# Kernel optimization log

Hardware: AMD Instinct MI355X
Metric: run time of the kernel (lower is better)

## Reference

```python
import jax, jax.numpy as jnp
import numpy as np

N, E = 50000, 800000
F_IN, HID, HEADS, OUT = 128, 32, 4, 16
NEG_SLOPE = 0.2  # PyG GATConv default leaky_relu slope


def segment_softmax(logits, seg, n):
    # numerically stable softmax over edges grouped by destination node
    m = jax.ops.segment_max(logits, seg, num_segments=n)          # [N,H]
    m = jnp.where(jnp.isfinite(m), m, 0.0)                        # guard empty segments
    e = jnp.exp(logits - m[seg])                                  # [E,H]
    s = jax.ops.segment_sum(e, seg, num_segments=n)               # [N,H]
    return e / (s[seg] + 1e-16)


def gat_conv(x, W, a_src, a_dst, bias, src, dst, concat):
    H, C = a_src.shape
    n = x.shape[0]
    h = (x @ W).reshape(n, H, C)                                  # [N,H,C]
    alpha_src = jnp.einsum('nhc,hc->nh', h, a_src)                # [N,H]
    alpha_dst = jnp.einsum('nhc,hc->nh', h, a_dst)                # [N,H]
    e = jax.nn.leaky_relu(alpha_src[src] + alpha_dst[dst], NEG_SLOPE)  # [E,H]
    alpha = segment_softmax(e, dst, n)                            # [E,H]
    msg = h[src] * alpha[:, :, None]                              # [E,H,C]
    out = jax.ops.segment_sum(msg, dst, num_segments=n)           # [N,H,C]
    out = out.reshape(n, H * C) if concat else out.mean(axis=1)
    return out + bias


def setup_inputs() -> dict:
    key = jax.random.key(0)
    ks = jax.random.split(key, 12)
    s = 0.1  # keep attention logits in a sane range
    return {
        'x': jax.random.normal(ks[0], (N, F_IN), jnp.float32),
        'edge_index': jax.random.randint(ks[1], (2, E), 0, N),
        'Wemb': jax.random.normal(ks[2], (F_IN, HID), jnp.float32) * s,
        'bemb': jnp.zeros((HID,), jnp.float32),
        'W1': jax.random.normal(ks[3], (HID, HEADS * HID), jnp.float32) * s,
        'a_src1': jax.random.normal(ks[4], (HEADS, HID), jnp.float32) * s,
        'a_dst1': jax.random.normal(ks[5], (HEADS, HID), jnp.float32) * s,
        'b1': jnp.zeros((HEADS * HID,), jnp.float32),
        'W2': jax.random.normal(ks[6], (HEADS * HID, HEADS * OUT), jnp.float32) * s,
        'a_src2': jax.random.normal(ks[7], (HEADS, OUT), jnp.float32) * s,
        'a_dst2': jax.random.normal(ks[8], (HEADS, OUT), jnp.float32) * s,
        'b2': jnp.zeros((OUT,), jnp.float32),
    }


def reference(x, edge_index, Wemb, bemb, W1, a_src1, a_dst1, b1, W2, a_src2, a_dst2, b2):
    src, dst = edge_index[0], edge_index[1]
    h = x @ Wemb + bemb  # dropout layers are identity at inference
    h = jax.nn.elu(gat_conv(h, W1, a_src1, a_dst1, b1, src, dst, True))
    h = gat_conv(h, W2, a_src2, a_dst2, b2, src, dst, False)
    return jax.nn.log_softmax(h, axis=1)
```

## Files before the change

kernel.cpp:

```cpp
#include <hip/hip_runtime.h>

#define N_NODES 50000
#define N_EDGES 800000
#define F_IN    128
#define HID     32
#define HEADS   4
#define OUT_C   16

#define NBKT 196
#define CAP  5120
#define EPB  4096
#define NB64 782

typedef __attribute__((ext_vector_type(8))) short bf16x8;
typedef __attribute__((ext_vector_type(4))) float f32x4;

__device__ __forceinline__ unsigned short f2bf(float f) {
    unsigned int u = __float_as_uint(f);
    u += 0x7FFFu + ((u >> 16) & 1u);
    return (unsigned short)(u >> 16);
}
__device__ __forceinline__ float bf_lo(unsigned int u) { return __uint_as_float(u << 16); }
__device__ __forceinline__ float bf_hi(unsigned int u) { return __uint_as_float(u & 0xFFFF0000u); }
__device__ __forceinline__ float bf2f(unsigned short s) {
    return __uint_as_float(((unsigned int)s) << 16);
}

__device__ __forceinline__ float edge_w(float asv, float adv) {
    float v = asv + adv;
    v = (v > 0.f) ? v : 0.2f * v;
    return __expf(v);
}

__global__ __launch_bounds__(256) void k_F1(const float* __restrict__ x,
                                            const float* __restrict__ Wemb,
                                            const float* __restrict__ bemb,
                                            const float* __restrict__ W1,
                                            const float* __restrict__ a_src,
                                            const float* __restrict__ a_dst,
                                            unsigned short* __restrict__ h0b,
                                            float* __restrict__ as, float* __restrict__ ad,
                                            const int* __restrict__ ei,
                                            int* __restrict__ gcnt,
                                            unsigned int* __restrict__ pairs) {
    __shared__ unsigned short xsb[64][136];
    __shared__ unsigned short wet[HID][136];
    __shared__ float bl[HID];
    __shared__ float vs[HID][4];
    __shared__ float vd[HID][4];
    __shared__ int hist[NBKT];
    __shared__ int base[NBKT];
    int t = threadIdx.x;
    if (blockIdx.x < NB64) {
        int node0 = blockIdx.x * 64;
        if (t < HID) bl[t] = bemb[t];
        {
            int k = (t & 127) >> 2, h = t & 3;
            const float* wrow = W1 + k * 128 + h * 32;
            const float* arow = ((t < 128) ? a_src : a_dst) + h * 32;
            float accv = 0.f;
            #pragma unroll
            for (int c2 = 0; c2 < 32; c2++) accv += wrow[c2] * arow[c2];
            if (t < 128) vs[k][h] = accv; else vd[k][h] = accv;
        }
        #pragma unroll
        for (int it = 0; it < 4; it++) {
            int idx = it * 256 + t;
            int k = idx >> 3, c4 = idx & 7;
            float4 w = *(const float4*)(Wemb + k * HID + c4 * 4);
            wet[c4 * 4 + 0][k] = f2bf(w.x);
            wet[c4 * 4 + 1][k] = f2bf(w.y);
            wet[c4 * 4 + 2][k] = f2bf(w.z);
            wet[c4 * 4 + 3][k] = f2bf(w.w);
        }
        #pragma unroll
        for (int it = 0; it < 8; it++) {
            int idx = it * 256 + t;
            int row = idx >> 5, c4 = idx & 31;
            float4 v = make_float4(0.f, 0.f, 0.f, 0.f);
            if (node0 + row < N_NODES) v = *(const float4*)(x + (size_t)(node0 + row) * F_IN + c4 * 4);
            ushort4 b;
            b.x = f2bf(v.x); b.y = f2bf(v.y); b.z = f2bf(v.z); b.w = f2bf(v.w);
            *(ushort4*)&xsb[row][c4 * 4] = b;
        }
        __syncthreads();
        int lane = t & 63, wv = t >> 6;
        int lrow = lane & 15, lk = lane >> 4;
        const char* abase = (const char*)&xsb[wv * 16 + lrow][0];
        f32x4 o[2];
        #pragma unroll
        for (int nt = 0; nt < 2; nt++) {
            f32x4 z = {};
            #pragma unroll
            for (int kt = 0; kt < 4; kt++) {
                bf16x8 af = *(const bf16x8*)(abase + kt * 64 + lk * 16);
                bf16x8 bfr = *(const bf16x8*)((const char*)&wet[nt * 16 + lrow][0] + kt * 64 + lk * 16);
                z = __builtin_amdgcn_mfma_f32_16x16x32_bf16(af, bfr, z, 0, 0, 0);
            }
            o[nt] = z;
        }
        float b0 = bl[lrow], b1v = bl[16 + lrow];
        float vsl[2][4], vdl[2][4];
        #pragma unroll
        for (int h = 0; h < 4; h++) {
            vsl[0][h] = vs[lrow][h];      vsl[1][h] = vs[16 + lrow][h];
            vdl[0][h] = vd[lrow][h];      vdl[1][h] = vd[16 + lrow][h];
        }
        #pragma unroll
        for (int r = 0; r < 4; r++) {
            int node = node0 + wv * 16 + lk * 4 + r;
            float h0v0 = o[0][r] + b0;
            float h0v1 = o[1][r] + b1v;
            if (node < N_NODES) {
                h0b[(size_t)node * HID + lrow]      = f2bf(h0v0);
                h0b[(size_t)node * HID + 16 + lrow] = f2bf(h0v1);
            }
            float p[4], qd[4];
            #pragma unroll
            for (int h = 0; h < 4; h++) {
                p[h]  = h0v0 * vsl[0][h] + h0v1 * vsl[1][h];
                qd[h] = h0v0 * vdl[0][h] + h0v1 * vdl[1][h];
            }
            #pragma unroll
            for (int mask = 1; mask <= 8; mask <<= 1) {
                #pragma unroll
                for (int h = 0; h < 4; h++) {
                    p[h]  += __shfl_xor(p[h],  mask, 64);
                    qd[h] += __shfl_xor(qd[h], mask, 64);
                }
            }
            if (lrow == 0 && node < N_NODES) {
                *(float4*)(as + node * 4) = make_float4(p[0], p[1], p[2], p[3]);
                *(float4*)(ad + node * 4) = make_float4(qd[0], qd[1], qd[2], qd[3]);
            }
        }
    } else {
        int e0 = (blockIdx.x - NB64) * EPB;
        for (int i = t; i < NBKT; i += 256) hist[i] = 0;
        __syncthreads();
        unsigned int p[16];
        int bb[16];
        #pragma unroll
        for (int i = 0; i < 16; i++) {
            int e = e0 + i * 256 + t;
            bb[i] = -1;
            if (e < N_EDGES) {
                int s = ei[e], d = ei[N_EDGES + e];
                p[i] = ((unsigned int)s << 8) | (unsigned int)(d & 255);
                bb[i] = d >> 8;
                atomicAdd(&hist[bb[i]], 1);
            }
        }
        __syncthreads();
        for (int i = t; i < NBKT; i += 256) {
            int c = hist[i];
            base[i] = i * CAP + (c ? atomicAdd(&gcnt[i], c) : 0);
            hist[i] = 0;
        }
        __syncthreads();
        #pragma unroll
        for (int i = 0; i < 16; i++) {
            if (bb[i] >= 0) {
                int off = atomicAdd(&hist[bb[i]], 1);
                pairs[base[bb[i]] + off] = p[i];
            }
        }
    }
}

__global__ __launch_bounds__(256) void k_F2(const unsigned int* __restrict__ pairs,
                                            const int* __restrict__ gcnt,
                                            int* __restrict__ rowptr,
                                            int* __restrict__ esrc) {
    __shared__ int cnt[256];
    __shared__ int cur[256];
    __shared__ int wsum[4];
    int t = threadIdx.x;
    int b = blockIdx.x;
    int lane = t & 63, wv = t >> 6;
    int v0 = (t < NBKT && t < b) ? gcnt[t] : 0;
    #pragma unroll
    for (int mask = 1; mask < 64; mask <<= 1) v0 += __shfl_xor(v0, mask, 64);
    if (lane == 0) wsum[wv] = v0;
    __syncthreads();
    int base = wsum[0] + wsum[1] + wsum[2] + wsum[3];
    int n0 = b << 8;
    int cntb = gcnt[b];
    int s0 = b * CAP;
    cnt[t] = 0;
    __syncthreads();
    for (int i = t; i < cntb; i += 256) atomicAdd(&cnt[pairs[s0 + i] & 255], 1);
    __syncthreads();
    int v = cnt[t], x = v;
    #pragma unroll
    for (int off = 1; off < 64; off <<= 1) { int y = __shfl_up(x, off, 64); if (lane >= off) x += y; }
    __syncthreads();
    if (lane == 63) wsum[wv] = x;
    __syncthreads();
    int add = 0;
    for (int j = 0; j < wv; j++) add += wsum[j];
    int excl = base + (x - v) + add;
    cur[t] = excl;
    if (n0 + t < N_NODES) rowptr[n0 + t] = excl;
    if (b == 0 && t == 0) rowptr[N_NODES] = N_EDGES;
    __syncthreads();
    for (int i = t; i < cntb; i += 256) {
        unsigned int p = pairs[s0 + i];
        int pos = atomicAdd(&cur[p & 255], 1);
        esrc[pos] = (int)(p >> 8);
    }
}

__global__ __launch_bounds__(256) void k_gather1(const int* __restrict__ esrc,
                                                 const int* __restrict__ rowptr,
                                                 const unsigned int* __restrict__ h0b,
                                                 const float* __restrict__ as,
                                                 const float* __restrict__ ad,
                                                 unsigned int* __restrict__ awb) {
    int t = threadIdx.x;
    int node = blockIdx.x * 4 + (t >> 6);
    int lane = t & 63;
    int head = lane >> 4;
    int cp = lane & 15;
    int s16 = lane >> 2;
    int h4 = lane & 3;
    int lb = cp * 4;
    int hb = head * 4;
    int beg = rowptr[node], end = rowptr[node + 1];
    float ad_w = ad[node * 4 + h4];
    float ax = 0.f, ay = 0.f, s = 0.f;
    const char* hc = (const char*)h0b;
    for (int k = beg; k < end; k += 16) {
        int idx = k + s16;
        int sm = esrc[min(idx, end - 1)];
#define G1L(J) int sj##J = __builtin_amdgcn_readlane(sm, (J) * 4); \
        unsigned int u##J = *(const unsigned int*)(hc + (size_t)(unsigned)sj##J * 64 + lb);
        G1L(0)  G1L(1)  G1L(2)  G1L(3)  G1L(4)  G1L(5)  G1L(6)  G1L(7)
        G1L(8)  G1L(9)  G1L(10) G1L(11) G1L(12) G1L(13) G1L(14) G1L(15)
#undef G1L
        float wm = edge_w(as[sm * 4 + h4], ad_w);
        if (idx >= end) wm = 0.f;
        int wmi = __float_as_int(wm);
#define G1W(J) float w##J = __int_as_float(__builtin_amdgcn_ds_bpermute(hb + (J) * 16, wmi));
        G1W(0)  G1W(1)  G1W(2)  G1W(3)  G1W(4)  G1W(5)  G1W(6)  G1W(7)
        G1W(8)  G1W(9)  G1W(10) G1W(11) G1W(12) G1W(13) G1W(14) G1W(15)
#undef G1W
        ax += bf_lo(u0)  * w0  + bf_lo(u1)  * w1  + bf_lo(u2)  * w2  + bf_lo(u3)  * w3
            + bf_lo(u4)  * w4  + bf_lo(u5)  * w5  + bf_lo(u6)  * w6  + bf_lo(u7)  * w7
            + bf_lo(u8)  * w8  + bf_lo(u9)  * w9  + bf_lo(u10) * w10 + bf_lo(u11) * w11
            + bf_lo(u12) * w12 + bf_lo(u13) * w13 + bf_lo(u14) * w14 + bf_lo(u15) * w15;
        ay += bf_hi(u0)  * w0  + bf_hi(u1)  * w1  + bf_hi(u2)  * w2  + bf_hi(u3)  * w3
            + bf_hi(u4)  * w4  + bf_hi(u5)  * w5  + bf_hi(u6)  * w6  + bf_hi(u7)  * w7
            + bf_hi(u8)  * w8  + bf_hi(u9)  * w9  + bf_hi(u10) * w10 + bf_hi(u11) * w11
            + bf_hi(u12) * w12 + bf_hi(u13) * w13 + bf_hi(u14) * w14 + bf_hi(u15) * w15;
        s += (w0 + w1 + w2 + w3) + (w4 + w5 + w6 + w7)
           + (w8 + w9 + w10 + w11) + (w12 + w13 + w14 + w15);
    }
    float rs = 1.0f / (s + 1e-16f);
    awb[(size_t)node * 64 + lane] = ((unsigned int)f2bf(ay * rs) << 16) | (unsigned int)f2bf(ax * rs);
}

__global__ __launch_bounds__(256) void k_h12(const unsigned int* __restrict__ awb,
                                             const float* __restrict__ W1,
                                             const float* __restrict__ b1,
                                             const float* __restrict__ W2,
                                             const float* __restrict__ a_src,
                                             const float* __restrict__ a_dst,
                                             unsigned short* __restrict__ h2,
                                             float* __restrict__ as, float* __restrict__ ad) {
    __shared__ unsigned int xsu[64][68];
    __shared__ unsigned short w1t[128][40];
    __shared__ unsigned short w2t[64][136];
    __shared__ float b1s[128];
    int t = threadIdx.x;
    int node0 = blockIdx.x * 64;
    if (t < 128) b1s[t] = b1[t];
    #pragma unroll
    for (int it = 0; it < 4; it++) {
        int idx = it * 256 + t;
        int row = idx >> 4, c4 = idx & 15;
        uint4 v = make_uint4(0u, 0u, 0u, 0u);
        if (node0 + row < N_NODES) v = *(const uint4*)(awb + (size_t)(node0 + row) * 64 + c4 * 4);
        *(uint4*)&xsu[row][c4 * 4] = v;
    }
    #pragma unroll
    for (int it = 0; it < 16; it++) {
        int idx = it * 256 + t;
        int k = idx >> 7, n = idx & 127;
        w1t[n][k] = f2bf(W1[idx]);
    }
    #pragma unroll
    for (int it = 0; it < 8; it++) {
        int idx = it * 256 + t;
        int k = idx >> 4, n4 = idx & 15;
        float4 w = *(const float4*)(W2 + k * 64 + n4 * 4);
        w2t[n4 * 4 + 0][k] = f2bf(w.x);
        w2t[n4 * 4 + 1][k] = f2bf(w.y);
        w2t[n4 * 4 + 2][k] = f2bf(w.z);
        w2t[n4 * 4 + 3][k] = f2bf(w.w);
    }
    __syncthreads();
    int lane = t & 63, wv = t >> 6;
    int lrow = lane & 15, lk = lane >> 4;
    const char* abase = (const char*)&xsu[wv * 16 + lrow][0];
    f32x4 o1[8];
    #pragma unroll
    for (int nt = 0; nt < 8; nt++) {
        int kt = nt >> 1;
        bf16x8 af = *(const bf16x8*)(abase + kt * 64 + lk * 16);
        bf16x8 bf1 = *(const bf16x8*)((const char*)&w1t[nt * 16 + lrow][0] + lk * 16);
        f32x4 z = {};
        o1[nt] = __builtin_amdgcn_mfma_f32_16x16x32_bf16(af, bf1, z, 0, 0, 0);
    }
    __syncthreads();
    unsigned short* o1t = (unsigned short*)&xsu[0][0];
    #pragma unroll
    for (int nt = 0; nt < 8; nt++) {
        float bb = b1s[nt * 16 + lrow];
        #pragma unroll
        for (int r = 0; r < 4; r++) {
            int noderow = wv * 16 + lk * 4 + r;
            float v = o1[nt][r] + bb;
            v = (v > 0.f) ? v : (__expf(v) - 1.0f);
            o1t[noderow * 136 + nt * 16 + lrow] = f2bf(v);
        }
    }
    __syncthreads();
    f32x4 acc[4] = {};
    const char* xbase = (const char*)&o1t[(wv * 16 + lrow) * 136];
    #pragma unroll
    for (int kt = 0; kt < 4; kt++) {
        bf16x8 af = *(const bf16x8*)(xbase + kt * 64 + lk * 16);
        #pragma unroll
        for (int h = 0; h < 4; h++) {
            bf16x8 bfr = *(const bf16x8*)((const char*)&w2t[h * 16 + lrow][0] + kt * 64 + lk * 16);
            acc[h] = __builtin_amdgcn_mfma_f32_16x16x32_bf16(af, bfr, acc[h], 0, 0, 0);
        }
    }
    float av[4], dv[4];
    #pragma unroll
    for (int h = 0; h < 4; h++) { av[h] = a_src[h * 16 + lrow]; dv[h] = a_dst[h * 16 + lrow]; }
    #pragma unroll
    for (int r = 0; r < 4; r++) {
        int node = node0 + wv * 16 + lk * 4 + r;
        float psh[4], pdh[4];
        #pragma unroll
        for (int h = 0; h < 4; h++) {
            float v = acc[h][r];
            if (node < N_NODES) h2[(size_t)node * 64 + h * 16 + lrow] = f2bf(v);
            float p = v * av[h], qv = v * dv[h];
            #pragma unroll
            for (int mask = 1; mask < 16; mask <<= 1) {
                p += __shfl_xor(p, mask, 64);
                qv += __shfl_xor(qv, mask, 64);
            }
            psh[h] = p; pdh[h] = qv;
        }
        if (lrow == 0 && node < N_NODES) {
            *(float4*)(as + node * 4) = make_float4(psh[0], psh[1], psh[2], psh[3]);
            *(float4*)(ad + node * 4) = make_float4(pdh[0], pdh[1], pdh[2], pdh[3]);
        }
    }
}

__global__ __launch_bounds__(256) void k_gather2(const int* __restrict__ esrc,
                                                 const int* __restrict__ rowptr,
                                                 const unsigned short* __restrict__ h2,
                                                 const float* __restrict__ as,
                                                 const float* __restrict__ ad,
                                                 const float* __restrict__ b2,
                                                 float* __restrict__ out) {
    int t = threadIdx.x;
    int node = blockIdx.x * 4 + (t >> 6);
    int lane = t & 63;
    int head = lane >> 4, c = lane & 15;
    int s16 = lane >> 2;
    int h4 = lane & 3;
    int lb = lane * 2;
    int hb = head * 4;
    int beg = rowptr[node], end = rowptr[node + 1];
    float ad_w = ad[node * 4 + h4];
    float acc = 0.f, s = 0.f;
    const char* h2c = (const char*)h2;
    for (int k = beg; k < end; k += 16) {
        int idx = k + s16;
        int sm = esrc[min(idx, end - 1)];
#define G2L(J) int sj##J = __builtin_amdgcn_readlane(sm, (J) * 4); \
        float r##J = bf2f(*(const unsigned short*)(h2c + (size_t)(unsigned)sj##J * 128 + lb));
        G2L(0)  G2L(1)  G2L(2)  G2L(3)  G2L(4)  G2L(5)  G2L(6)  G2L(7)
        G2L(8)  G2L(9)  G2L(10) G2L(11) G2L(12) G2L(13) G2L(14) G2L(15)
#undef G2L
        float wm = edge_w(as[sm * 4 + h4], ad_w);
        if (idx >= end) wm = 0.f;
        int wmi = __float_as_int(wm);
#define G2W(J) float w##J = __int_as_float(__builtin_amdgcn_ds_bpermute(hb + (J) * 16, wmi));
        G2W(0)  G2W(1)  G2W(2)  G2W(3)  G2W(4)  G2W(5)  G2W(6)  G2W(7)
        G2W(8)  G2W(9)  G2W(10) G2W(11) G2W(12) G2W(13) G2W(14) G2W(15)
#undef G2W
        acc += r0 * w0 + r1 * w1 + r2 * w2 + r3 * w3
             + r4 * w4 + r5 * w5 + r6 * w6 + r7 * w7
             + r8 * w8 + r9 * w9 + r10 * w10 + r11 * w11
             + r12 * w12 + r13 * w13 + r14 * w14 + r15 * w15;
        s += (w0 + w1 + w2 + w3) + (w4 + w5 + w6 + w7)
           + (w8 + w9 + w10 + w11) + (w12 + w13 + w14 + w15);
    }
    float v = acc * (1.0f / (s + 1e-16f));
    v += __shfl_xor(v, 16, 64);
    v += __shfl_xor(v, 32, 64);
    v = v * 0.25f + b2[c];
    float m = v;
    #pragma unroll
    for (int mask = 1; mask < 16; mask <<= 1) m = fmaxf(m, __shfl_xor(m, mask, 64));
    float ex = __expf(v - m);
    float se = ex;
    #pragma unroll
    for (int mask = 1; mask < 16; mask <<= 1) se += __shfl_xor(se, mask, 64);
    float res = (v - m) - __logf(se);
    if (lane < 16) out[(size_t)node * 16 + lane] = res;
}

extern "C" void kernel_launch(void* const* d_in, const int* in_sizes, int n_in,
                              void* d_out, int out_size, void* d_ws, size_t ws_size,
                              hipStream_t stream) {
    const float* x      = (const float*)d_in[0];
    const int*   ei     = (const int*)d_in[1];
    const float* Wemb   = (const float*)d_in[2];
    const float* bemb   = (const float*)d_in[3];
    const float* W1     = (const float*)d_in[4];
    const float* a_src1 = (const float*)d_in[5];
    const float* a_dst1 = (const float*)d_in[6];
    const float* b1     = (const float*)d_in[7];
    const float* W2     = (const float*)d_in[8];
    const float* a_src2 = (const float*)d_in[9];
    const float* a_dst2 = (const float*)d_in[10];
    const float* b2     = (const float*)d_in[11];
    float* out = (float*)d_out;

    char* ws = (char*)d_ws;
    size_t off = 0;
    auto alloc = [&](size_t bytes) { char* p = ws + off; off += (bytes + 255) & ~size_t(255); return p; };
    unsigned short* h2b   = (unsigned short*)alloc((size_t)N_NODES * 64 * 2);
    unsigned int*   awb   = (unsigned int*)alloc((size_t)N_NODES * 64 * 4);
    unsigned short* h0b = (unsigned short*)alloc((size_t)N_NODES * HID * 2);
    int*          esrc  = (int*)alloc((size_t)N_EDGES * 4 + 64);
    unsigned int* pairs = (unsigned int*)alloc((size_t)NBKT * CAP * 4);
    float* as     = (float*)alloc((size_t)N_NODES * 4 * 4);
    float* ad     = (float*)alloc((size_t)N_NODES * 4 * 4);
    int*   rowptr = (int*)alloc((size_t)(N_NODES + 1) * 4);
    int*   gcnt   = (int*)alloc((size_t)NBKT * 4);

    const int GB = N_NODES / 4;

    hipMemsetAsync(gcnt, 0, (size_t)NBKT * 4, stream);
    k_F1<<<NB64 + NBKT, 256, 0, stream>>>(x, Wemb, bemb, W1, a_src1, a_dst1,
                                          h0b, as, ad, ei, gcnt, pairs);
    k_F2<<<NBKT, 256, 0, stream>>>(pairs, gcnt, rowptr, esrc);
    k_gather1<<<GB, 256, 0, stream>>>(esrc, rowptr, (const unsigned int*)h0b, as, ad, awb);
    k_h12<<<NB64, 256, 0, stream>>>(awb, W1, b1, W2, a_src2, a_dst2, h2b, as, ad);
    k_gather2<<<GB, 256, 0, stream>>>(esrc, rowptr, h2b, as, ad, b2, out);
}
```

Measured before the change: 190.4 us.

## Store layer-2 features head-major and gather one head at a time

The second-layer projection is now written head-major ([head][node][16] in bf16), so each head's features for a node are a contiguous 32-byte row. The layer-2 aggregation kernel loops over the four heads. Each lane handles one edge and a 4-channel quarter, loading 8 bytes per gathered source, and the partial sums are combined with cross-lane shuffles. This replaces the old scheme of 16 scalar 2-byte loads per lane with readlane and bpermute weight broadcasts, aiming for wider, better-coalesced gathers and less cross-lane traffic. In exchange the edge list and source attention scores are read four times, once per head.

After: 221.6 us. 1.16x slower.

```diff
diff --git a/kernel.cpp b/kernel.cpp
--- a/kernel.cpp
+++ b/kernel.cpp
@@ -266,7 +266,7 @@
                                              const float* __restrict__ W2,
                                              const float* __restrict__ a_src,
                                              const float* __restrict__ a_dst,
-                                             unsigned short* __restrict__ h2,
+                                             unsigned short* __restrict__ h2hm,
                                              float* __restrict__ as, float* __restrict__ ad) {
     __shared__ unsigned int xsu[64][68];
     __shared__ unsigned short w1t[128][40];
@@ -347,7 +347,7 @@
         #pragma unroll
         for (int h = 0; h < 4; h++) {
             float v = acc[h][r];
-            if (node < N_NODES) h2[(size_t)node * 64 + h * 16 + lrow] = f2bf(v);
+            if (node < N_NODES) h2hm[((size_t)h * N_NODES + node) * 16 + lrow] = f2bf(v);
             float p = v * av[h], qv = v * dv[h];
             #pragma unroll
             for (int mask = 1; mask < 16; mask <<= 1) {
@@ -365,7 +365,7 @@
 
 __global__ __launch_bounds__(256) void k_gather2(const int* __restrict__ esrc,
                                                  const int* __restrict__ rowptr,
-                                                 const unsigned short* __restrict__ h2,
+                                                 const unsigned short* __restrict__ h2hm,
                                                  const float* __restrict__ as,
                                                  const float* __restrict__ ad,
                                                  const float* __restrict__ b2,
@@ -373,50 +373,53 @@
     int t = threadIdx.x;
     int node = blockIdx.x * 4 + (t >> 6);
     int lane = t & 63;
-    int head = lane >> 4, c = lane & 15;
-    int s16 = lane >> 2;
-    int h4 = lane & 3;
-    int lb = lane * 2;
-    int hb = head * 4;
+    int s = lane >> 2;
+    int q = lane & 3;
     int beg = rowptr[node], end = rowptr[node + 1];
-    float ad_w = ad[node * 4 + h4];
-    float acc = 0.f, s = 0.f;
-    const char* h2c = (const char*)h2;
-    for (int k = beg; k < end; k += 16) {
-        int idx = k + s16;
-        int sm = esrc[min(idx, end - 1)];
-#define G2L(J) int sj##J = __builtin_amdgcn_readlane(sm, (J) * 4); \
-        float r##J = bf2f(*(const unsigned short*)(h2c + (size_t)(unsigned)sj##J * 128 + lb));
-        G2L(0)  G2L(1)  G2L(2)  G2L(3)  G2L(4)  G2L(5)  G2L(6)  G2L(7)
-        G2L(8)  G2L(9)  G2L(10) G2L(11) G2L(12) G2L(13) G2L(14) G2L(15)
-#undef G2L
-        float wm = edge_w(as[sm * 4 + h4], ad_w);
-        if (idx >= end) wm = 0.f;
-        int wmi = __float_as_int(wm);
-#define G2W(J) float w##J = __int_as_float(__builtin_amdgcn_ds_bpermute(hb + (J) * 16, wmi));
-        G2W(0)  G2W(1)  G2W(2)  G2W(3)  G2W(4)  G2W(5)  G2W(6)  G2W(7)
-        G2W(8)  G2W(9)  G2W(10) G2W(11) G2W(12) G2W(13) G2W(14) G2W(15)
-#undef G2W
-        acc += r0 * w0 + r1 * w1 + r2 * w2 + r3 * w3
-             + r4 * w4 + r5 * w5 + r6 * w6 + r7 * w7
-             + r8 * w8 + r9 * w9 + r10 * w10 + r11 * w11
-             + r12 * w12 + r13 * w13 + r14 * w14 + r15 * w15;
-        s += (w0 + w1 + w2 + w3) + (w4 + w5 + w6 + w7)
-           + (w8 + w9 + w10 + w11) + (w12 + w13 + w14 + w15);
-    }
-    float v = acc * (1.0f / (s + 1e-16f));
-    v += __shfl_xor(v, 16, 64);
-    v += __shfl_xor(v, 32, 64);
-    v = v * 0.25f + b2[c];
-    float m = v;
-    #pragma unroll
-    for (int mask = 1; mask < 16; mask <<= 1) m = fmaxf(m, __shfl_xor(m, mask, 64));
-    float ex = __expf(v - m);
-    float se = ex;
-    #pragma unroll
-    for (int mask = 1; mask < 16; mask <<= 1) se += __shfl_xor(se, mask, 64);
-    float res = (v - m) - __logf(se);
-    if (lane < 16) out[(size_t)node * 16 + lane] = res;
+    float4 adv = *(const float4*)(ad + node * 4);
+    float oa0 = 0.f, oa1 = 0.f, oa2 = 0.f, oa3 = 0.f;
+    const char* pc = (const char*)h2hm;
+    #pragma unroll
+    for (int hp = 0; hp < 4; hp++) {
+        float ad_w = (hp == 0) ? adv.x : (hp == 1) ? adv.y : (hp == 2) ? adv.z : adv.w;
+        const char* base = pc + (size_t)hp * N_NODES * 32;
+        float a0 = 0.f, a1 = 0.f, a2 = 0.f, a3 = 0.f, sacc = 0.f;
+        for (int k = beg; k < end; k += 16) {
+            int idx = k + s;
+            int sm = esrc[min(idx, end - 1)];
+            float wm = edge_w(as[sm * 4 + hp], ad_w);
+            if (idx >= end) wm = 0.f;
+            sacc += wm;
+            uint2 u = *(const uint2*)(base + (size_t)(unsigned)sm * 32 + q * 8);
+            a0 += bf_lo(u.x) * wm;
+            a1 += bf_hi(u.x) * wm;
+            a2 += bf_lo(u.y) * wm;
+            a3 += bf_hi(u.y) * wm;
+        }
+        #pragma unroll
+        for (int m = 4; m <= 32; m <<= 1) {
+            sacc += __shfl_xor(sacc, m, 64);
+            a0 += __shfl_xor(a0, m, 64);
+            a1 += __shfl_xor(a1, m, 64);
+            a2 += __shfl_xor(a2, m, 64);
+            a3 += __shfl_xor(a3, m, 64);
+        }
+        float rs = 0.25f / (sacc + 1e-16f);
+        oa0 += a0 * rs; oa1 += a1 * rs; oa2 += a2 * rs; oa3 += a3 * rs;
+    }
+    float4 b2v = *(const float4*)(b2 + q * 4);
+    float v0 = oa0 + b2v.x, v1 = oa1 + b2v.y, v2 = oa2 + b2v.z, v3 = oa3 + b2v.w;
+    float m = fmaxf(fmaxf(v0, v1), fmaxf(v2, v3));
+    m = fmaxf(m, __shfl_xor(m, 1, 64));
+    m = fmaxf(m, __shfl_xor(m, 2, 64));
+    float se = __expf(v0 - m) + __expf(v1 - m) + __expf(v2 - m) + __expf(v3 - m);
+    se += __shfl_xor(se, 1, 64);
+    se += __shfl_xor(se, 2, 64);
+    float ls = __logf(se);
+    if (lane < 4) {
+        float4 o = make_float4(v0 - m - ls, v1 - m - ls, v2 - m - ls, v3 - m - ls);
+        *(float4*)(out + (size_t)node * 16 + q * 4) = o;
+    }
 }
 
 extern "C" void kernel_launch(void* const* d_in, const int* in_sizes, int n_in,
```
